# Optimization experiments

Hardware: AMD Instinct MI355X
Metric: run time of the kernel (lower is better)

Reference implementation:

```python
import jax, jax.numpy as jnp
import numpy as np
from itertools import permutations

B, S, D = 1024, 16, 128
G_DIMS = [256, 256]
F_DIMS = [256, 256]

# all ordered pairs (i, j), i != j, in the same lexicographic order as
# itertools.permutations used by the torch module
_PAIRS = np.array(list(permutations(range(S), 2)), dtype=np.int32)  # [P, 2], P = S*(S-1)


def _init_linear(key, in_dim, out_dim):
    kw, kb = jax.random.split(key)
    bound = 1.0 / np.sqrt(in_dim)
    W = jax.random.uniform(kw, (in_dim, out_dim), jnp.float32, -bound, bound)
    b = jax.random.uniform(kb, (out_dim,), jnp.float32, -bound, bound)
    return W, b


def setup_inputs() -> dict:
    key = jax.random.key(0)
    ks = jax.random.split(key, 5)
    state = jax.random.normal(ks[0], (B, S, D), jnp.float32)
    gW0, gb0 = _init_linear(ks[1], 2 * D, G_DIMS[0])
    gW1, gb1 = _init_linear(ks[2], G_DIMS[0], G_DIMS[1])
    fW0, fb0 = _init_linear(ks[3], G_DIMS[1], F_DIMS[0])
    fW1, fb1 = _init_linear(ks[4], F_DIMS[0], F_DIMS[1])
    return {"state": state,
            "gW0": gW0, "gb0": gb0, "gW1": gW1, "gb1": gb1,
            "fW0": fW0, "fb0": fb0, "fW1": fW1, "fb1": fb1}


def reference(state, gW0, gb0, gW1, gb1, fW0, fb0, fW1, fb1):
    i_idx = jnp.asarray(_PAIRS[:, 0])
    j_idx = jnp.asarray(_PAIRS[:, 1])
    # gather + concat all ordered pairs: [B, P, 2D]
    paired = jnp.concatenate([state[:, i_idx], state[:, j_idx]], axis=-1)
    # g-MLP applied per pair
    h = jax.nn.relu(jnp.einsum('bpd,de->bpe', paired, gW0) + gb0)
    h = jax.nn.relu(jnp.einsum('bpd,de->bpe', h, gW1) + gb1)
    # sum over pairs -> [B, g_out]
    pooled = h.sum(axis=1)
    # f-MLP
    out = jax.nn.relu(pooled @ fW0 + fb0)
    out = jax.nn.relu(out @ fW1 + fb1)
    return out
```

## Files before the change

kernel.cpp:

```cpp
#include <hip/hip_runtime.h>

typedef __attribute__((ext_vector_type(8))) _Float16 f16x8;
typedef __attribute__((ext_vector_type(4))) float f32x4;

#define HSTR 264

__global__ __launch_bounds__(256) void prep_kernel(
    const float* __restrict__ gW0, const float* __restrict__ gW1,
    _Float16* __restrict__ W0c, _Float16* __restrict__ W1c)
{
  const int t = blockIdx.x * 256 + threadIdx.x;
  {
    const int c = t >> 7, k = t & 127;
    const int dst = ((k >> 5) * 32 + (c >> 4)) * 512 +
                    (((k >> 3) & 3) * 16 + (c & 15)) * 8 + (k & 7);
    const int src = (k + ((c >= 256) ? 128 : 0)) * 256 + (c & 255);
    W0c[dst] = (_Float16)gW0[src];
  }
  {
    const int n = t >> 8, k = t & 255;
    const int dst = ((k >> 5) * 16 + (n >> 4)) * 512 +
                    (((k >> 3) & 3) * 16 + (n & 15)) * 8 + (k & 7);
    W1c[dst] = (_Float16)gW1[k * 256 + n];
  }
}

__global__ __launch_bounds__(512, 4) void pair_kernel(
    const float* __restrict__ state,
    const _Float16* __restrict__ W0c, const float* __restrict__ gb0,
    const _Float16* __restrict__ W1c, const float* __restrict__ gb1,
    float* __restrict__ pooled)
{
  const int b   = blockIdx.x;
  const int tid = threadIdx.x;
  const int w   = tid >> 6;
  const int l   = tid & 63;
  const int lr  = l & 15;
  const int lg  = l >> 4;

  __shared__ _Float16 A_lds[16 * HSTR];
  __shared__ _Float16 C_lds[16 * HSTR];

  const float* stb = state + (size_t)b * 2048;

  f16x8 sfrag[4];
  #pragma unroll
  for (int kk = 0; kk < 4; ++kk) {
    const float* sp = stb + lr * 128 + kk * 32 + lg * 8;
    f32x4 s0 = *(const f32x4*)sp;
    f32x4 s1 = *(const f32x4*)(sp + 4);
    f16x8 f;
    f[0] = (_Float16)s0[0]; f[1] = (_Float16)s0[1];
    f[2] = (_Float16)s0[2]; f[3] = (_Float16)s0[3];
    f[4] = (_Float16)s1[0]; f[5] = (_Float16)s1[1];
    f[6] = (_Float16)s1[2]; f[7] = (_Float16)s1[3];
    sfrag[kk] = f;
  }

  const f32x4 z4 = {0.f, 0.f, 0.f, 0.f};
  f32x4 acc2[4];
  #pragma unroll
  for (int nt = 0; nt < 4; ++nt) acc2[nt] = z4;

  #pragma unroll
  for (int nt = 0; nt < 4; ++nt) {
    #pragma unroll
    for (int kk = 0; kk < 4; ++kk) {
      f16x8 bf = *(const f16x8*)(W0c + (size_t)((kk * 32 + 4 * w + nt) * 512 + l * 8));
      acc2[nt] = __builtin_amdgcn_mfma_f32_16x16x32_f16(sfrag[kk], bf, acc2[nt], 0, 0, 0);
    }
  }

  #pragma unroll
  for (int nt = 0; nt < 4; ++nt) {
    const int col = 64 * w + 16 * nt + lr;
    #pragma unroll
    for (int r = 0; r < 4; ++r) {
      const int row = lg * 4 + r;
      const float v = acc2[nt][r];
      if (col < 256) A_lds[row * HSTR + col]       = (_Float16)(v + gb0[col]);
      else           C_lds[row * HSTR + col - 256] = (_Float16)v;
    }
  }
  __syncthreads();

  f16x8 creg[8];
  #pragma unroll
  for (int kk = 0; kk < 8; ++kk)
    creg[kk] = *(const f16x8*)&C_lds[lr * HSTR + kk * 32 + lg * 8];

  f16x8 bw[2][8];
  #pragma unroll
  for (int nt = 0; nt < 2; ++nt)
    #pragma unroll
    for (int kk = 0; kk < 8; ++kk)
      bw[nt][kk] = *(const f16x8*)(W1c + (size_t)((kk * 16 + 2 * w + nt) * 512 + l * 8));

  float gb1v[2];
  #pragma unroll
  for (int nt = 0; nt < 2; ++nt) gb1v[nt] = gb1[32 * w + 16 * nt + lr];

  const f16x8 zh = {(_Float16)0, (_Float16)0, (_Float16)0, (_Float16)0,
                    (_Float16)0, (_Float16)0, (_Float16)0, (_Float16)0};

  float pp[2] = {0.f, 0.f};
  #pragma unroll 1
  for (int i = 0; i < 16; ++i) {
    f32x4 acc0 = z4, acc1 = z4;
    #pragma unroll
    for (int kk = 0; kk < 8; ++kk) {
      f16x8 a = *(const f16x8*)&A_lds[i * HSTR + kk * 32 + lg * 8];
      f16x8 u = __builtin_elementwise_max(a + creg[kk], zh);
      acc0 = __builtin_amdgcn_mfma_f32_16x16x32_f16(u, bw[0][kk], acc0, 0, 0, 0);
      acc1 = __builtin_amdgcn_mfma_f32_16x16x32_f16(u, bw[1][kk], acc1, 0, 0, 0);
    }
    #pragma unroll
    for (int r = 0; r < 4; ++r) {
      const int row = lg * 4 + r;
      const float v0 = fmaxf(acc0[r] + gb1v[0], 0.f);
      const float v1 = fmaxf(acc1[r] + gb1v[1], 0.f);
      pp[0] += (row == i) ? 0.f : v0;
      pp[1] += (row == i) ? 0.f : v1;
    }
  }

  #pragma unroll
  for (int nt = 0; nt < 2; ++nt) {
    float v = pp[nt];
    v += __shfl_xor(v, 16);
    v += __shfl_xor(v, 32);
    if (lg == 0) pooled[(size_t)b * 256 + 32 * w + 16 * nt + lr] = v;
  }
}

__global__ __launch_bounds__(256) void fmlp_kernel(
    const float* __restrict__ pooled,
    const float* __restrict__ fW0, const float* __restrict__ fb0,
    const float* __restrict__ fW1, const float* __restrict__ fb1,
    float* __restrict__ out)
{
  const int tid = threadIdx.x;
  const size_t b0 = (size_t)blockIdx.x * 8;
  __shared__ float pl[8][256];
  __shared__ float h1[8][256];

  #pragma unroll
  for (int q = 0; q < 8; ++q) {
    const int idx = q * 256 + tid;
    pl[idx >> 8][idx & 255] = pooled[b0 * 256 + idx];
  }
  __syncthreads();

  float acc[8] = {0.f, 0.f, 0.f, 0.f, 0.f, 0.f, 0.f, 0.f};
  #pragma unroll 4
  for (int k = 0; k < 256; ++k) {
    const float wv = fW0[(size_t)k * 256 + tid];
    #pragma unroll
    for (int q = 0; q < 8; ++q) acc[q] = fmaf(pl[q][k], wv, acc[q]);
  }
  #pragma unroll
  for (int q = 0; q < 8; ++q) h1[q][tid] = fmaxf(acc[q] + fb0[tid], 0.f);
  __syncthreads();

  float acc2[8] = {0.f, 0.f, 0.f, 0.f, 0.f, 0.f, 0.f, 0.f};
  #pragma unroll 4
  for (int k = 0; k < 256; ++k) {
    const float wv = fW1[(size_t)k * 256 + tid];
    #pragma unroll
    for (int q = 0; q < 8; ++q) acc2[q] = fmaf(h1[q][k], wv, acc2[q]);
  }
  #pragma unroll
  for (int q = 0; q < 8; ++q)
    out[(b0 + q) * 256 + tid] = fmaxf(acc2[q] + fb1[tid], 0.f);
}

extern "C" void kernel_launch(void* const* d_in, const int* in_sizes, int n_in,
                              void* d_out, int out_size, void* d_ws, size_t ws_size,
                              hipStream_t stream) {
  const float* state = (const float*)d_in[0];
  const float* gW0   = (const float*)d_in[1];
  const float* gb0   = (const float*)d_in[2];
  const float* gW1   = (const float*)d_in[3];
  const float* gb1   = (const float*)d_in[4];
  const float* fW0   = (const float*)d_in[5];
  const float* fb0   = (const float*)d_in[6];
  const float* fW1   = (const float*)d_in[7];
  const float* fb1   = (const float*)d_in[8];
  float* out = (float*)d_out;

  _Float16* W0c = (_Float16*)d_ws;
  _Float16* W1c = W0c + 65536;
  float* pooled = (float*)(W1c + 65536);

  const int Bn = in_sizes[0] / 2048;

  prep_kernel<<<dim3(256), dim3(256), 0, stream>>>(gW0, gW1, W0c, W1c);
  pair_kernel<<<dim3(Bn), dim3(512), 0, stream>>>(state, W0c, gb0, W1c, gb1, pooled);
  fmlp_kernel<<<dim3(Bn / 8), dim3(256), 0, stream>>>(pooled, fW0, fb0, fW1, fb1, out);
}
```

Measured before the change: 75.49 us.

## Halve pair-kernel waves, pin W1 fragments in AGPRs with inline MFMA asm

Pair kernel now runs 4 waves per batch instead of 8, with each wave computing twice as many output column tiles in both GEMMs. The W1 fragments are held in accumulation registers and fed to hand-written MFMA inline asm with manual s_nop hazard padding, aiming to reuse each relu'd A fragment across four MFMAs and relieve VGPR pressure. The fmlp kernel processes 4 batches per block instead of 8, doubling its grid. Risks are hazard-timing errors in the manual asm, lower latency hiding from fewer waves, and lost compiler scheduling around the volatile asm.

```diff
diff --git a/kernel.cpp b/kernel.cpp
--- a/kernel.cpp
+++ b/kernel.cpp
@@ -25,7 +25,7 @@
   }
 }
 
-__global__ __launch_bounds__(512, 4) void pair_kernel(
+__global__ __launch_bounds__(256, 2) void pair_kernel(
     const float* __restrict__ state,
     const _Float16* __restrict__ W0c, const float* __restrict__ gb0,
     const _Float16* __restrict__ W1c, const float* __restrict__ gb1,
@@ -58,22 +58,22 @@
   }
 
   const f32x4 z4 = {0.f, 0.f, 0.f, 0.f};
-  f32x4 acc2[4];
-  #pragma unroll
-  for (int nt = 0; nt < 4; ++nt) acc2[nt] = z4;
-
-  #pragma unroll
-  for (int nt = 0; nt < 4; ++nt) {
+  f32x4 acc2[8];
+  #pragma unroll
+  for (int nt = 0; nt < 8; ++nt) acc2[nt] = z4;
+
+  #pragma unroll
+  for (int nt = 0; nt < 8; ++nt) {
     #pragma unroll
     for (int kk = 0; kk < 4; ++kk) {
-      f16x8 bf = *(const f16x8*)(W0c + (size_t)((kk * 32 + 4 * w + nt) * 512 + l * 8));
+      f16x8 bf = *(const f16x8*)(W0c + (size_t)((kk * 32 + 8 * w + nt) * 512 + l * 8));
       acc2[nt] = __builtin_amdgcn_mfma_f32_16x16x32_f16(sfrag[kk], bf, acc2[nt], 0, 0, 0);
     }
   }
 
   #pragma unroll
-  for (int nt = 0; nt < 4; ++nt) {
-    const int col = 64 * w + 16 * nt + lr;
+  for (int nt = 0; nt < 8; ++nt) {
+    const int col = 128 * w + 16 * nt + lr;
     #pragma unroll
     for (int r = 0; r < 4; ++r) {
       const int row = lg * 4 + r;
@@ -89,47 +89,62 @@
   for (int kk = 0; kk < 8; ++kk)
     creg[kk] = *(const f16x8*)&C_lds[lr * HSTR + kk * 32 + lg * 8];
 
-  f16x8 bw[2][8];
-  #pragma unroll
-  for (int nt = 0; nt < 2; ++nt)
-    #pragma unroll
-    for (int kk = 0; kk < 8; ++kk)
-      bw[nt][kk] = *(const f16x8*)(W1c + (size_t)((kk * 16 + 2 * w + nt) * 512 + l * 8));
-
-  float gb1v[2];
-  #pragma unroll
-  for (int nt = 0; nt < 2; ++nt) gb1v[nt] = gb1[32 * w + 16 * nt + lr];
+  f16x8 bw[4][8];
+  #pragma unroll
+  for (int nt = 0; nt < 4; ++nt) {
+    #pragma unroll
+    for (int kk = 0; kk < 8; ++kk) {
+      bw[nt][kk] = *(const f16x8*)(W1c + (size_t)((kk * 16 + 4 * w + nt) * 512 + l * 8));
+      asm volatile("" : "+a"(bw[nt][kk]));
+    }
+  }
+
+  float gb1v[4];
+  #pragma unroll
+  for (int nt = 0; nt < 4; ++nt) gb1v[nt] = gb1[64 * w + 16 * nt + lr];
 
   const f16x8 zh = {(_Float16)0, (_Float16)0, (_Float16)0, (_Float16)0,
                     (_Float16)0, (_Float16)0, (_Float16)0, (_Float16)0};
 
-  float pp[2] = {0.f, 0.f};
+  float pp[4] = {0.f, 0.f, 0.f, 0.f};
   #pragma unroll 1
   for (int i = 0; i < 16; ++i) {
-    f32x4 acc0 = z4, acc1 = z4;
+    f32x4 a0 = z4, a1 = z4, a2 = z4, a3 = z4;
     #pragma unroll
     for (int kk = 0; kk < 8; ++kk) {
-      f16x8 a = *(const f16x8*)&A_lds[i * HSTR + kk * 32 + lg * 8];
-      f16x8 u = __builtin_elementwise_max(a + creg[kk], zh);
-      acc0 = __builtin_amdgcn_mfma_f32_16x16x32_f16(u, bw[0][kk], acc0, 0, 0, 0);
-      acc1 = __builtin_amdgcn_mfma_f32_16x16x32_f16(u, bw[1][kk], acc1, 0, 0, 0);
-    }
+      f16x8 av = *(const f16x8*)&A_lds[i * HSTR + kk * 32 + lg * 8];
+      f16x8 u = __builtin_elementwise_max(av + creg[kk], zh);
+      asm volatile("s_nop 3\n\tv_mfma_f32_16x16x32_f16 %0, %1, %2, %0"
+                   : "+v"(a0) : "v"(u), "a"(bw[0][kk]));
+      asm volatile("v_mfma_f32_16x16x32_f16 %0, %1, %2, %0"
+                   : "+v"(a1) : "v"(u), "a"(bw[1][kk]));
+      asm volatile("v_mfma_f32_16x16x32_f16 %0, %1, %2, %0"
+                   : "+v"(a2) : "v"(u), "a"(bw[2][kk]));
+      asm volatile("v_mfma_f32_16x16x32_f16 %0, %1, %2, %0"
+                   : "+v"(a3) : "v"(u), "a"(bw[3][kk]));
+    }
+    asm volatile("s_nop 7\n\ts_nop 7");
+
     #pragma unroll
     for (int r = 0; r < 4; ++r) {
       const int row = lg * 4 + r;
-      const float v0 = fmaxf(acc0[r] + gb1v[0], 0.f);
-      const float v1 = fmaxf(acc1[r] + gb1v[1], 0.f);
+      const float v0 = fmaxf(a0[r] + gb1v[0], 0.f);
+      const float v1 = fmaxf(a1[r] + gb1v[1], 0.f);
+      const float v2 = fmaxf(a2[r] + gb1v[2], 0.f);
+      const float v3 = fmaxf(a3[r] + gb1v[3], 0.f);
       pp[0] += (row == i) ? 0.f : v0;
       pp[1] += (row == i) ? 0.f : v1;
-    }
-  }
-
-  #pragma unroll
-  for (int nt = 0; nt < 2; ++nt) {
+      pp[2] += (row == i) ? 0.f : v2;
+      pp[3] += (row == i) ? 0.f : v3;
+    }
+  }
+
+  #pragma unroll
+  for (int nt = 0; nt < 4; ++nt) {
     float v = pp[nt];
     v += __shfl_xor(v, 16);
     v += __shfl_xor(v, 32);
-    if (lg == 0) pooled[(size_t)b * 256 + 32 * w + 16 * nt + lr] = v;
+    if (lg == 0) pooled[(size_t)b * 256 + 64 * w + 16 * nt + lr] = v;
   }
 }
 
@@ -140,37 +155,35 @@
     float* __restrict__ out)
 {
   const int tid = threadIdx.x;
-  const size_t b0 = (size_t)blockIdx.x * 8;
-  __shared__ float pl[8][256];
-  __shared__ float h1[8][256];
-
-  #pragma unroll
-  for (int q = 0; q < 8; ++q) {
-    const int idx = q * 256 + tid;
-    pl[idx >> 8][idx & 255] = pooled[b0 * 256 + idx];
-  }
+  const size_t b0 = (size_t)blockIdx.x * 4;
+  __shared__ float pl[4][256];
+  __shared__ float h1[4][256];
+
+  #pragma unroll
+  for (int q = 0; q < 4; ++q)
+    pl[q][tid] = pooled[(b0 + q) * 256 + tid];
   __syncthreads();
 
-  float acc[8] = {0.f, 0.f, 0.f, 0.f, 0.f, 0.f, 0.f, 0.f};
-  #pragma unroll 4
+  float acc[4] = {0.f, 0.f, 0.f, 0.f};
+  #pragma unroll 8
   for (int k = 0; k < 256; ++k) {
     const float wv = fW0[(size_t)k * 256 + tid];
     #pragma unroll
-    for (int q = 0; q < 8; ++q) acc[q] = fmaf(pl[q][k], wv, acc[q]);
-  }
-  #pragma unroll
-  for (int q = 0; q < 8; ++q) h1[q][tid] = fmaxf(acc[q] + fb0[tid], 0.f);
+    for (int q = 0; q < 4; ++q) acc[q] = fmaf(pl[q][k], wv, acc[q]);
+  }
+  #pragma unroll
+  for (int q = 0; q < 4; ++q) h1[q][tid] = fmaxf(acc[q] + fb0[tid], 0.f);
   __syncthreads();
 
-  float acc2[8] = {0.f, 0.f, 0.f, 0.f, 0.f, 0.f, 0.f, 0.f};
-  #pragma unroll 4
+  float acc2[4] = {0.f, 0.f, 0.f, 0.f};
+  #pragma unroll 8
   for (int k = 0; k < 256; ++k) {
     const float wv = fW1[(size_t)k * 256 + tid];
     #pragma unroll
-    for (int q = 0; q < 8; ++q) acc2[q] = fmaf(h1[q][k], wv, acc2[q]);
-  }
-  #pragma unroll
-  for (int q = 0; q < 8; ++q)
+    for (int q = 0; q < 4; ++q) acc2[q] = fmaf(h1[q][k], wv, acc2[q]);
+  }
+  #pragma unroll
+  for (int q = 0; q < 4; ++q)
     out[(b0 + q) * 256 + tid] = fmaxf(acc2[q] + fb1[tid], 0.f);
 }
 
@@ -195,6 +208,6 @@
   const int Bn = in_sizes[0] / 2048;
 
   prep_kernel<<<dim3(256), dim3(256), 0, stream>>>(gW0, gW1, W0c, W1c);
-  pair_kernel<<<dim3(Bn), dim3(512), 0, stream>>>(state, W0c, gb0, W1c, gb1, pooled);
-  fmlp_kernel<<<dim3(Bn / 8), dim3(256), 0, stream>>>(pooled, fW0, fb0, fW1, fb1, out);
-}
+  pair_kernel<<<dim3(Bn), dim3(256), 0, stream>>>(state, W0c, gb0, W1c, gb1, pooled);
+  fmlp_kernel<<<dim3(Bn / 4), dim3(256), 0, stream>>>(pooled, fW0, fb0, fW1, fb1, out);
+}
```

Result: slower. 78.00 us (+3.3%).
